# Performance work log

Measured on AMD Instinct MI355X. Metric: run time of the kernel, lower is better.

The kernel has to match this reference:

```python
import jax, jax.numpy as jnp
import numpy as np

B, S, HID = 2, 1024, 1024
H, P, D = 16, 2, 64
SCALE = 1.0 / np.sqrt(D)


def setup_inputs() -> dict:
    key = jax.random.key(0)
    ks = jax.random.split(key, 9)
    hidden_states = jax.random.normal(ks[0], (B, S, HID), dtype=jnp.float32)
    w_std = 0.02
    Wq = jax.random.normal(ks[1], (HID, HID), dtype=jnp.float32) * w_std
    Wk = jax.random.normal(ks[2], (HID, HID), dtype=jnp.float32) * w_std
    Wv = jax.random.normal(ks[3], (HID, HID), dtype=jnp.float32) * w_std
    Wo = jax.random.normal(ks[4], (HID, HID), dtype=jnp.float32) * w_std
    # alpha_* initialized as identity over heads, broadcast over pseudo dim, plus noise
    ident = jnp.broadcast_to(jnp.eye(H, dtype=jnp.float32)[:, :, None], (H, H, P))
    alpha_q = ident + 0.01 * jax.random.normal(ks[5], (H, H, P), dtype=jnp.float32)
    alpha_k = ident + 0.01 * jax.random.normal(ks[6], (H, H, P), dtype=jnp.float32)
    alpha_v = ident + 0.01 * jax.random.normal(ks[7], (H, H, P), dtype=jnp.float32)
    # collapse: (H, H*P), one-hot picking pseudo-head 0 of each head, plus noise
    collapse = jnp.zeros((H, H * P), dtype=jnp.float32)
    hi = jnp.arange(H)
    collapse = collapse.at[hi, hi * P].set(1.0)
    collapse = collapse + 0.01 * jax.random.normal(ks[8], (H, H * P), dtype=jnp.float32)
    return {"hidden_states": hidden_states, "Wq": Wq, "Wk": Wk, "Wv": Wv, "Wo": Wo,
            "alpha_q": alpha_q, "alpha_k": alpha_k, "alpha_v": alpha_v, "collapse": collapse}


def _iha_forward(x, Wq, Wk, Wv, Wo, alpha_q, alpha_k, alpha_v, collapse):
    b, s, _ = x.shape
    # projections (torch F.linear: x @ W^T), split into heads -> (b, H, s, D)
    def proj(W):
        return jnp.einsum('bse,fe->bsf', x, W).reshape(b, s, H, D).transpose(0, 2, 1, 3)
    q, k, v = proj(Wq), proj(Wk), proj(Wv)
    # head mixing: mhp,bmnd->bhpnd then merge pseudo into virtual seq (b,H,s*P,D)
    def mix_merge(alpha, t):
        t = jnp.einsum('mhp,bmnd->bhpnd', alpha, t)
        return t.transpose(0, 1, 3, 2, 4).reshape(b, H, s * P, D)
    q, k, v = mix_merge(alpha_q, q), mix_merge(alpha_k, k), mix_merge(alpha_v, v)
    # causal SDPA over virtual positions
    sv = s * P
    scores = jnp.einsum('bhqd,bhkd->bhqk', q, k) * jnp.asarray(SCALE, x.dtype)
    vpos = jnp.arange(sv)
    causal = vpos[:, None] >= vpos[None, :]
    scores = jnp.where(causal, scores, jnp.asarray(-jnp.inf, x.dtype))
    probs = jax.nn.softmax(scores, axis=-1)
    attn = jnp.einsum('bhqk,bhkd->bhqd', probs, v)  # (b, H, sv, D)
    # collapse pseudo heads: (b,H,s,P,D) -> (b,s,H*P,D) -> einsum with collapse
    attn = attn.reshape(b, H, s, P, D).transpose(0, 2, 1, 3, 4).reshape(b, s, H * P, D)
    attn = jnp.einsum('ho,bnod->bhnd', collapse, attn)  # (b, H, s, D)
    attn = attn.transpose(0, 2, 1, 3).reshape(b, s, HID)
    return jnp.einsum('bse,fe->bsf', attn, Wo)


def reference(hidden_states, Wq, Wk, Wv, Wo, alpha_q, alpha_k, alpha_v, collapse):
    return _iha_forward(hidden_states, Wq, Wk, Wv, Wo, alpha_q, alpha_k, alpha_v, collapse)
```

## Files before the change

### kernel.cpp

```cpp
#include <hip/hip_runtime.h>
#include <hip/hip_bf16.h>

#define B_    2
#define S_    1024
#define HID_  1024
#define H_    16
#define P_    2
#define D_    64
#define SV_   2048
#define NBH_  32
#define SCALE_LOG2E 0.18033688f

typedef __attribute__((ext_vector_type(8))) short short8;
typedef __attribute__((ext_vector_type(4))) short short4b;
typedef __attribute__((ext_vector_type(4))) float f32x4;

#if __has_builtin(__builtin_amdgcn_exp2f)
#define EXP2(x) __builtin_amdgcn_exp2f(x)
#else
#define EXP2(x) exp2f(x)
#endif

__device__ __forceinline__ unsigned short f2bf(float f) {
  union { float f; unsigned u; } v; v.f = f;
  unsigned r = v.u + 0x7fffu + ((v.u >> 16) & 1u);
  return (unsigned short)(r >> 16);
}
__device__ __forceinline__ unsigned pack_bf2(float a, float b) {
  __hip_bfloat162 h = __float22bfloat162_rn(make_float2(a, b));
  unsigned u; __builtin_memcpy(&u, &h, 4);
  return u;
}

__global__ __launch_bounds__(256) void prep_kernel(
    const float* __restrict__ x,
    const float* __restrict__ Wq, const float* __restrict__ Wk,
    const float* __restrict__ Wv, const float* __restrict__ Wo,
    const float* __restrict__ aq, const float* __restrict__ ak,
    const float* __restrict__ av, const float* __restrict__ coll,
    unsigned short* __restrict__ Xb, unsigned short* __restrict__ Weff,
    unsigned short* __restrict__ Woeff) {
  __shared__ float shbuf[1536];
  const int bid = blockIdx.x;
  const int tid = threadIdx.x;

  if (bid < 1024) {
    const int n4 = (B_ * S_ * HID_) / 4;
    int i = bid * 256 + tid;
    const int stride = 1024 * 256;
    for (; i < n4; i += stride) {
      float4 v = ((const float4*)x)[i];
      ushort4 o;
      o.x = f2bf(v.x); o.y = f2bf(v.y); o.z = f2bf(v.z); o.w = f2bf(v.w);
      ((ushort4*)Xb)[i] = o;
    }
  } else if (bid < 1216) {
    const int wb = bid - 1024;
    const int d = wb & 63;
    const int t = wb >> 6;
    const float* W = (t == 0) ? Wq : ((t == 1) ? Wk : Wv);
    const float* A = (t == 0) ? aq : ((t == 1) ? ak : av);
    float (*Al)[32] = (float (*)[32])shbuf;
    for (int idx = tid; idx < 512; idx += 256) Al[idx >> 5][idx & 31] = A[idx];
    __syncthreads();
    const int e = tid * 4;
    float wr[16][4];
#pragma unroll
    for (int m = 0; m < 16; ++m) {
      float4 v = *(const float4*)(W + (size_t)(m * 64 + d) * 1024 + e);
      wr[m][0] = v.x; wr[m][1] = v.y; wr[m][2] = v.z; wr[m][3] = v.w;
    }
    for (int hp = 0; hp < 32; ++hp) {
      float acc0 = 0.f, acc1 = 0.f, acc2 = 0.f, acc3 = 0.f;
#pragma unroll
      for (int m = 0; m < 16; ++m) {
        float al = Al[m][hp];
        acc0 += al * wr[m][0]; acc1 += al * wr[m][1];
        acc2 += al * wr[m][2]; acc3 += al * wr[m][3];
      }
      int r = (hp >> 1) * 128 + (hp & 1) * 64 + d;
      ushort4 ov;
      ov.x = f2bf(acc0); ov.y = f2bf(acc1); ov.z = f2bf(acc2); ov.w = f2bf(acc3);
      *(ushort4*)(Weff + ((size_t)t * 2048 + r) * 1024 + e) = ov;
    }
  } else {
    const int f = bid - 1216;
    float* wrow = shbuf;
    float* cl = shbuf + 1024;
    for (int idx = tid; idx < 512; idx += 256) cl[idx] = coll[idx];
    for (int idx = tid; idx < 1024; idx += 256) wrow[idx] = Wo[(size_t)f * 1024 + idx];
    __syncthreads();
    for (int idx = tid; idx < 2048; idx += 256) {
      int o = idx >> 6, d = idx & 63;
      float acc = 0.f;
#pragma unroll
      for (int h = 0; h < 16; ++h) acc += wrow[h * 64 + d] * cl[h * 32 + o];
      Woeff[(size_t)f * 2048 + idx] = f2bf(acc);
    }
  }
}

__global__ __launch_bounds__(256, 3) void qkv_gemm128(
    const unsigned short* __restrict__ Xb,
    const unsigned short* __restrict__ Weff,
    unsigned short* __restrict__ Qd, unsigned short* __restrict__ Kd,
    unsigned short* __restrict__ Vd) {
  __shared__ unsigned short As[3][128 * 32];
  __shared__ unsigned short Bs[3][128 * 32];
  constexpr int K = 1024, NT = 32;
  const int t = threadIdx.x;
  const int wave = t >> 6, lane = t & 63, lq = lane & 15, quad = lane >> 4;
  const int wm = wave >> 1, wn = wave & 1;
  const int z = blockIdx.z;
  const int row0 = blockIdx.x * 128, col0 = blockIdx.y * 128;
  const unsigned short* Ap = (z == 2) ? (Weff + (size_t)2 * 2048 * 1024) : Xb;
  const unsigned short* Bp = (z == 2) ? Xb : (Weff + (size_t)z * 2048 * 1024);

  const int srow = lane >> 2;
  const int sgr = (lane & 3) ^ ((lane >> 3) & 3);

  auto stage = [&](int kt, int buf) {
#pragma unroll
    for (int j = 0; j < 2; ++j) {
      const int rloc = wave * 32 + j * 16;
      const unsigned short* ga =
          Ap + (size_t)(row0 + rloc + srow) * K + kt * 32 + sgr * 8;
      __builtin_amdgcn_global_load_lds(
          (const __attribute__((address_space(1))) unsigned int*)ga,
          (__attribute__((address_space(3))) unsigned int*)(&As[buf][rloc * 32]),
          16, 0, 0);
      const unsigned short* gb =
          Bp + (size_t)(col0 + rloc + srow) * K + kt * 32 + sgr * 8;
      __builtin_amdgcn_global_load_lds(
          (const __attribute__((address_space(1))) unsigned int*)gb,
          (__attribute__((address_space(3))) unsigned int*)(&Bs[buf][rloc * 32]),
          16, 0, 0);
    }
  };

  f32x4 acc[4][4];
#pragma unroll
  for (int mi = 0; mi < 4; ++mi)
#pragma unroll
    for (int ni = 0; ni < 4; ++ni) acc[mi][ni] = (f32x4){0.f, 0.f, 0.f, 0.f};

  stage(0, 0);
  stage(1, 1);

  const int swz4 = (lq >> 1) & 3;

  for (int kt = 0; kt < NT; ++kt) {
    const int buf = kt % 3;
    if (kt + 1 < NT) {
      asm volatile("s_waitcnt vmcnt(4)" ::: "memory");
    } else {
      asm volatile("s_waitcnt vmcnt(0)" ::: "memory");
    }
    asm volatile("s_barrier" ::: "memory");
    if (kt + 2 < NT) stage(kt + 2, (kt + 2) % 3);

    const unsigned short* __restrict__ Ab = &As[buf][0];
    const unsigned short* __restrict__ Bb = &Bs[buf][0];
    short8 af[4], bf[4];
#pragma unroll
    for (int mi = 0; mi < 4; ++mi)
      af[mi] = *(const short8*)(
          Ab + (wm * 64 + mi * 16 + lq) * 32 + ((quad ^ swz4) * 8));
#pragma unroll
    for (int ni = 0; ni < 4; ++ni)
      bf[ni] = *(const short8*)(
          Bb + (wn * 64 + ni * 16 + lq) * 32 + ((quad ^ swz4) * 8));
    __builtin_amdgcn_s_setprio(1);
#pragma unroll
    for (int mi = 0; mi < 4; ++mi)
#pragma unroll
      for (int ni = 0; ni < 4; ++ni)
        acc[mi][ni] = __builtin_amdgcn_mfma_f32_16x16x32_bf16(
            af[mi], bf[ni], acc[mi][ni], 0, 0, 0);
    __builtin_amdgcn_s_setprio(0);
  }

#pragma unroll
  for (int mi = 0; mi < 4; ++mi) {
#pragma unroll
    for (int ni = 0; ni < 4; ++ni) {
#pragma unroll
      for (int i = 0; i < 4; ++i) {
        int grow = row0 + wm * 64 + mi * 16 + quad * 4 + i;
        int gcol = col0 + wn * 64 + ni * 16 + lq;
        float val = acc[mi][ni][i];
        if (z != 2) {
          if (z == 0) val *= SCALE_LOG2E;
          int b = grow >> 10, n = grow & 1023;
          int h = gcol >> 7, p = (gcol >> 6) & 1, d = gcol & 63;
          unsigned short* dst = (z == 0) ? Qd : Kd;
          dst[((size_t)((b * 16 + h) * 2048) + n * 2 + p) * 64 + d] = f2bf(val);
        } else {
          int h = grow >> 7, p = (grow >> 6) & 1, d = grow & 63;
          int b = gcol >> 10, n = gcol & 1023;
          Vd[((size_t)((b * 16 + h) * 64 + d)) * 2048 + n * 2 + p] = f2bf(val);
        }
      }
    }
  }
}

__global__ __launch_bounds__(256) void gemm64p(
    const unsigned short* __restrict__ A,
    const unsigned short* __restrict__ Bbase,
    float* __restrict__ Cf) {
  __shared__ unsigned short As[3][64 * 64];
  __shared__ unsigned short Bs[3][64 * 64];
  constexpr int K = 2048, N = 1024, NT = 32;
  const int t = threadIdx.x;
  const int wave = t >> 6, lane = t & 63, lrow = lane & 15, quad = lane >> 4;
  const int wm = wave >> 1, wn = wave & 1;
  const int row0 = blockIdx.x * 64, col0 = blockIdx.y * 64;
  const int srow8 = lane >> 3;
  const int sslot = (lane & 7) ^ srow8;
  const int swz = lrow & 7;

  auto stage = [&](int kt, int buf) {
#pragma unroll
    for (int j = 0; j < 2; ++j) {
      const int rloc = wave * 16 + j * 8;
      const unsigned short* ga =
          A + (size_t)(row0 + rloc + srow8) * K + kt * 64 + sslot * 8;
      __builtin_amdgcn_global_load_lds(
          (const __attribute__((address_space(1))) unsigned int*)ga,
          (__attribute__((address_space(3))) unsigned int*)(&As[buf][rloc * 64]),
          16, 0, 0);
      const unsigned short* gb =
          Bbase + (size_t)(col0 + rloc + srow8) * K + kt * 64 + sslot * 8;
      __builtin_amdgcn_global_load_lds(
          (const __attribute__((address_space(1))) unsigned int*)gb,
          (__attribute__((address_space(3))) unsigned int*)(&Bs[buf][rloc * 64]),
          16, 0, 0);
    }
  };

  f32x4 acc[2][2];
#pragma unroll
  for (int mi = 0; mi < 2; ++mi)
#pragma unroll
    for (int ni = 0; ni < 2; ++ni) acc[mi][ni] = (f32x4){0.f, 0.f, 0.f, 0.f};

  stage(0, 0);
  stage(1, 1);

  for (int kt = 0; kt < NT; ++kt) {
    const int buf = kt % 3;
    if (kt < NT - 1) {
      asm volatile("s_waitcnt vmcnt(4)" ::: "memory");
    } else {
      asm volatile("s_waitcnt vmcnt(0)" ::: "memory");
    }
    asm volatile("s_barrier" ::: "memory");
    if (kt + 2 < NT) stage(kt + 2, (kt + 2) % 3);

    const unsigned short* __restrict__ Ab = &As[buf][0];
    const unsigned short* __restrict__ Bb = &Bs[buf][0];
    short8 af[2][2], bf[2][2];
#pragma unroll
    for (int mi = 0; mi < 2; ++mi)
#pragma unroll
      for (int ks = 0; ks < 2; ++ks)
        af[mi][ks] = *(const short8*)(
            Ab + (wm * 32 + mi * 16 + lrow) * 64 + (((ks * 4 + quad) ^ swz) * 8));
#pragma unroll
    for (int ni = 0; ni < 2; ++ni)
#pragma unroll
      for (int ks = 0; ks < 2; ++ks)
        bf[ni][ks] = *(const short8*)(
            Bb + (wn * 32 + ni * 16 + lrow) * 64 + (((ks * 4 + quad) ^ swz) * 8));
    __builtin_amdgcn_s_setprio(1);
#pragma unroll
    for (int mi = 0; mi < 2; ++mi)
#pragma unroll
      for (int ni = 0; ni < 2; ++ni) {
        acc[mi][ni] = __builtin_amdgcn_mfma_f32_16x16x32_bf16(
            af[mi][0], bf[ni][0], acc[mi][ni], 0, 0, 0);
        acc[mi][ni] = __builtin_amdgcn_mfma_f32_16x16x32_bf16(
            af[mi][1], bf[ni][1], acc[mi][ni], 0, 0, 0);
      }
    __builtin_amdgcn_s_setprio(0);
  }

#pragma unroll
  for (int mi = 0; mi < 2; ++mi)
#pragma unroll
    for (int ni = 0; ni < 2; ++ni)
#pragma unroll
      for (int i = 0; i < 4; ++i) {
        int grow = row0 + wm * 32 + mi * 16 + quad * 4 + i;
        int gcol = col0 + wn * 32 + ni * 16 + lrow;
        Cf[(size_t)grow * N + gcol] = acc[mi][ni][i];
      }
}

__global__ __launch_bounds__(256, 3) void attn_kernel(
    const unsigned short* __restrict__ Qv, const unsigned short* __restrict__ Kv,
    const unsigned short* __restrict__ Vt, unsigned short* __restrict__ Aov) {
  __shared__ unsigned short Ks[3][4096];
  __shared__ unsigned short Vs[3][4096];
  const int bh = blockIdx.x;
  const int yy = blockIdx.y;
  const int qt = (yy < 16) ? yy : (47 - yy);
  const int t = threadIdx.x;
  const int w = t >> 6, lane = t & 63, lq = lane & 15, quad = lane >> 4;
  const int l3 = lq & 7;

  const unsigned short* Qh = Qv + (size_t)bh * SV_ * D_;
  const unsigned short* Kh = Kv + (size_t)bh * SV_ * D_;
  const unsigned short* Vh = Vt + (size_t)bh * D_ * SV_;

  const int qrow = qt * 64 + w * 16 + lq;
  short8 bq0 = *(const short8*)(Qh + (size_t)qrow * 64 + quad * 8);
  short8 bq1 = *(const short8*)(Qh + (size_t)qrow * 64 + 32 + quad * 8);

  const int sg = (lane & 7) ^ ((lane >> 3) & 7);
  const int r0 = w * 16 + (lane >> 3);
  const unsigned short* Kg0 = Kh + r0 * 64 + sg * 8;
  const unsigned short* Vg0 = Vh + (size_t)r0 * SV_ + sg * 8;
  const int lds0 = w * 1024;
  const int lds1 = lds0 + 512;

  auto stage = [&](int kt) {
    const int buf = kt % 3;
    const unsigned short* kg = Kg0 + kt * 4096;
    const unsigned short* vg = Vg0 + kt * 64;
    __builtin_amdgcn_global_load_lds(
        (const __attribute__((address_space(1))) unsigned int*)kg,
        (__attribute__((address_space(3))) unsigned int*)(&Ks[buf][lds0]), 16, 0, 0);
    __builtin_amdgcn_global_load_lds(
        (const __attribute__((address_space(1))) unsigned int*)(kg + 8 * 64),
        (__attribute__((address_space(3))) unsigned int*)(&Ks[buf][lds1]), 16, 0, 0);
    __builtin_amdgcn_global_load_lds(
        (const __attribute__((address_space(1))) unsigned int*)vg,
        (__attribute__((address_space(3))) unsigned int*)(&Vs[buf][lds0]), 16, 0, 0);
    __builtin_amdgcn_global_load_lds(
        (const __attribute__((address_space(1))) unsigned int*)(vg + (size_t)8 * SV_),
        (__attribute__((address_space(3))) unsigned int*)(&Vs[buf][lds1]), 16, 0, 0);
  };

  float l_sum = 0.f;
  f32x4 o_acc[4];
#pragma unroll
  for (int nd = 0; nd < 4; ++nd) o_acc[nd] = (f32x4){0.f, 0.f, 0.f, 0.f};

  const int nt = qt + 1;
  stage(0);
  if (nt > 1) stage(1);

  for (int kt = 0; kt < nt; ++kt) {
    const int buf = kt % 3;
    if (kt + 1 < nt) {
      asm volatile("s_waitcnt vmcnt(4)" ::: "memory");
    } else {
      asm volatile("s_waitcnt vmcnt(0)" ::: "memory");
    }
    asm volatile("s_barrier" ::: "memory");
    if (kt + 2 < nt) stage(kt + 2);

    const unsigned short* Kb = Ks[buf];
    short8 ka[4][2];
#pragma unroll
    for (int t4 = 0; t4 < 4; ++t4)
#pragma unroll
      for (int c = 0; c < 2; ++c)
        ka[t4][c] = *(const short8*)(Kb + (t4 * 16 + lq) * 64 + (((c * 4 + quad) ^ l3) * 8));

    f32x4 s[4];
#pragma unroll
    for (int t4 = 0; t4 < 4; ++t4) {
      f32x4 z = (f32x4){0.f, 0.f, 0.f, 0.f};
      z = __builtin_amdgcn_mfma_f32_16x16x32_bf16(ka[t4][0], bq0, z, 0, 0, 0);
      s[t4] = __builtin_amdgcn_mfma_f32_16x16x32_bf16(ka[t4][1], bq1, z, 0, 0, 0);
    }

    const bool diag = (kt == qt);
    const int kc0 = kt * 64 + quad * 4;
    const unsigned short* Vb = Vs[buf];
    float rs = 0.f;
    __builtin_amdgcn_s_setprio(1);
#pragma unroll
    for (int t4 = 0; t4 < 4; ++t4) {
      float p0 = EXP2(s[t4][0]), p1 = EXP2(s[t4][1]);
      float p2 = EXP2(s[t4][2]), p3 = EXP2(s[t4][3]);
      if (diag) {
        const int kc = kc0 + t4 * 16;
        if (kc + 0 > qrow) p0 = 0.f;
        if (kc + 1 > qrow) p1 = 0.f;
        if (kc + 2 > qrow) p2 = 0.f;
        if (kc + 3 > qrow) p3 = 0.f;
      }
      rs += (p0 + p1) + (p2 + p3);
      unsigned ww[2];
      ww[0] = pack_bf2(p0, p1);
      ww[1] = pack_bf2(p2, p3);
      short4b pb;
      __builtin_memcpy(&pb, ww, 8);
      const int cg = t4 * 2 + (quad >> 1);
      const int vcol = ((cg ^ l3) * 8) + (quad & 1) * 4;
#pragma unroll
      for (int nd = 0; nd < 4; ++nd) {
        short4b va4;
        __builtin_memcpy(&va4, Vb + (nd * 16 + lq) * 64 + vcol, 8);
        o_acc[nd] = __builtin_amdgcn_mfma_f32_16x16x16bf16_1k(va4, pb,
                                                              o_acc[nd], 0, 0, 0);
      }
    }
    __builtin_amdgcn_s_setprio(0);
    l_sum += rs;
  }

  l_sum += __shfl_xor(l_sum, 16);
  l_sum += __shfl_xor(l_sum, 32);

  const int b = bh >> 4, h = bh & 15;
  const float inv = 1.0f / l_sum;
  const int n = qrow >> 1, p = qrow & 1;
  unsigned short* dst = Aov + ((size_t)(b * 1024 + n)) * 2048 + (h * 2 + p) * 64;
#pragma unroll
  for (int nd = 0; nd < 4; ++nd) {
    uint2 dw;
    dw.x = pack_bf2(o_acc[nd][0] * inv, o_acc[nd][1] * inv);
    dw.y = pack_bf2(o_acc[nd][2] * inv, o_acc[nd][3] * inv);
    *(uint2*)(dst + nd * 16 + quad * 4) = dw;
  }
}

extern "C" void kernel_launch(void* const* d_in, const int* in_sizes, int n_in,
                              void* d_out, int out_size, void* d_ws, size_t ws_size,
                              hipStream_t stream) {
  (void)in_sizes; (void)n_in; (void)out_size; (void)ws_size;
  const float* x    = (const float*)d_in[0];
  const float* Wq   = (const float*)d_in[1];
  const float* Wk   = (const float*)d_in[2];
  const float* Wv   = (const float*)d_in[3];
  const float* Wo   = (const float*)d_in[4];
  const float* aq   = (const float*)d_in[5];
  const float* ak   = (const float*)d_in[6];
  const float* av   = (const float*)d_in[7];
  const float* coll = (const float*)d_in[8];
  float* out = (float*)d_out;

  char* ws = (char*)d_ws;
  const size_t MB = 1024 * 1024;
  unsigned short* Xb    = (unsigned short*)(ws);
  unsigned short* Woeff = (unsigned short*)(ws + 4 * MB);
  unsigned short* Weff  = (unsigned short*)(ws + 8 * MB);
  unsigned short* Qv    = (unsigned short*)(ws + 20 * MB);
  unsigned short* Kv    = (unsigned short*)(ws + 28 * MB);
  unsigned short* Vt    = (unsigned short*)(ws + 36 * MB);
  unsigned short* Aov   = (unsigned short*)(ws + 8 * MB);

  prep_kernel<<<dim3(2240), dim3(256), 0, stream>>>(
      x, Wq, Wk, Wv, Wo, aq, ak, av, coll, Xb, Weff, Woeff);
  qkv_gemm128<<<dim3(16, 16, 3), dim3(256), 0, stream>>>(Xb, Weff, Qv, Kv, Vt);
  attn_kernel<<<dim3(32, 32), dim3(256), 0, stream>>>(Qv, Kv, Vt, Aov);
  gemm64p<<<dim3(32, 16), dim3(256), 0, stream>>>(Aov, Woeff, out);
}
```

Baseline: 189.1 us.

## Process two query tiles per attention block to reuse staged K/V

Each attention workgroup now handles 128 query rows (two 64-row tiles) instead of 64, so every K/V tile staged into LDS feeds two sets of score and PV MFMAs. The grid is halved and the causal tile mapping is adjusted to match. The aim is to cut global-to-LDS traffic and barrier overhead per unit of work. In exchange, register pressure roughly doubles for the accumulators (launch bounds lowered to 2 waves per SIMD), there are half as many blocks to balance across CUs, and the first tile does a skipped extra iteration.

```diff
diff --git a/kernel.cpp b/kernel.cpp
--- a/kernel.cpp
+++ b/kernel.cpp
@@ -298,14 +298,14 @@
       }
 }
 
-__global__ __launch_bounds__(256, 3) void attn_kernel(
+__global__ __launch_bounds__(256, 2) void attn_kernel(
     const unsigned short* __restrict__ Qv, const unsigned short* __restrict__ Kv,
     const unsigned short* __restrict__ Vt, unsigned short* __restrict__ Aov) {
   __shared__ unsigned short Ks[3][4096];
   __shared__ unsigned short Vs[3][4096];
   const int bh = blockIdx.x;
   const int yy = blockIdx.y;
-  const int qt = (yy < 16) ? yy : (47 - yy);
+  const int qt = (yy < 8) ? yy : (23 - yy);
   const int t = threadIdx.x;
   const int w = t >> 6, lane = t & 63, lq = lane & 15, quad = lane >> 4;
   const int l3 = lq & 7;
@@ -314,9 +314,12 @@
   const unsigned short* Kh = Kv + (size_t)bh * SV_ * D_;
   const unsigned short* Vh = Vt + (size_t)bh * D_ * SV_;
 
-  const int qrow = qt * 64 + w * 16 + lq;
-  short8 bq0 = *(const short8*)(Qh + (size_t)qrow * 64 + quad * 8);
-  short8 bq1 = *(const short8*)(Qh + (size_t)qrow * 64 + 32 + quad * 8);
+  const int qrow0 = qt * 128 + w * 16 + lq;
+  const int qrow1 = qrow0 + 64;
+  short8 bq0_0 = *(const short8*)(Qh + (size_t)qrow0 * 64 + quad * 8);
+  short8 bq1_0 = *(const short8*)(Qh + (size_t)qrow0 * 64 + 32 + quad * 8);
+  short8 bq0_1 = *(const short8*)(Qh + (size_t)qrow1 * 64 + quad * 8);
+  short8 bq1_1 = *(const short8*)(Qh + (size_t)qrow1 * 64 + 32 + quad * 8);
 
   const int sg = (lane & 7) ^ ((lane >> 3) & 7);
   const int r0 = w * 16 + (lane >> 3);
@@ -343,14 +346,17 @@
         (__attribute__((address_space(3))) unsigned int*)(&Vs[buf][lds1]), 16, 0, 0);
   };
 
-  float l_sum = 0.f;
-  f32x4 o_acc[4];
-#pragma unroll
-  for (int nd = 0; nd < 4; ++nd) o_acc[nd] = (f32x4){0.f, 0.f, 0.f, 0.f};
-
-  const int nt = qt + 1;
+  float l_sum0 = 0.f, l_sum1 = 0.f;
+  f32x4 o_acc0[4], o_acc1[4];
+#pragma unroll
+  for (int nd = 0; nd < 4; ++nd) {
+    o_acc0[nd] = (f32x4){0.f, 0.f, 0.f, 0.f};
+    o_acc1[nd] = (f32x4){0.f, 0.f, 0.f, 0.f};
+  }
+
+  const int nt = 2 * qt + 2;
   stage(0);
-  if (nt > 1) stage(1);
+  stage(1);
 
   for (int kt = 0; kt < nt; ++kt) {
     const int buf = kt % 3;
@@ -370,63 +376,122 @@
       for (int c = 0; c < 2; ++c)
         ka[t4][c] = *(const short8*)(Kb + (t4 * 16 + lq) * 64 + (((c * 4 + quad) ^ l3) * 8));
 
-    f32x4 s[4];
-#pragma unroll
-    for (int t4 = 0; t4 < 4; ++t4) {
-      f32x4 z = (f32x4){0.f, 0.f, 0.f, 0.f};
-      z = __builtin_amdgcn_mfma_f32_16x16x32_bf16(ka[t4][0], bq0, z, 0, 0, 0);
-      s[t4] = __builtin_amdgcn_mfma_f32_16x16x32_bf16(ka[t4][1], bq1, z, 0, 0, 0);
-    }
-
-    const bool diag = (kt == qt);
+    const unsigned short* Vb = Vs[buf];
     const int kc0 = kt * 64 + quad * 4;
-    const unsigned short* Vb = Vs[buf];
-    float rs = 0.f;
     __builtin_amdgcn_s_setprio(1);
-#pragma unroll
-    for (int t4 = 0; t4 < 4; ++t4) {
-      float p0 = EXP2(s[t4][0]), p1 = EXP2(s[t4][1]);
-      float p2 = EXP2(s[t4][2]), p3 = EXP2(s[t4][3]);
-      if (diag) {
-        const int kc = kc0 + t4 * 16;
-        if (kc + 0 > qrow) p0 = 0.f;
-        if (kc + 1 > qrow) p1 = 0.f;
-        if (kc + 2 > qrow) p2 = 0.f;
-        if (kc + 3 > qrow) p3 = 0.f;
-      }
-      rs += (p0 + p1) + (p2 + p3);
-      unsigned ww[2];
-      ww[0] = pack_bf2(p0, p1);
-      ww[1] = pack_bf2(p2, p3);
-      short4b pb;
-      __builtin_memcpy(&pb, ww, 8);
-      const int cg = t4 * 2 + (quad >> 1);
-      const int vcol = ((cg ^ l3) * 8) + (quad & 1) * 4;
-#pragma unroll
-      for (int nd = 0; nd < 4; ++nd) {
-        short4b va4;
-        __builtin_memcpy(&va4, Vb + (nd * 16 + lq) * 64 + vcol, 8);
-        o_acc[nd] = __builtin_amdgcn_mfma_f32_16x16x16bf16_1k(va4, pb,
-                                                              o_acc[nd], 0, 0, 0);
-      }
-    }
+
+    if (kt <= 2 * qt) {
+      f32x4 s[4];
+#pragma unroll
+      for (int t4 = 0; t4 < 4; ++t4) {
+        f32x4 zz = (f32x4){0.f, 0.f, 0.f, 0.f};
+        zz = __builtin_amdgcn_mfma_f32_16x16x32_bf16(ka[t4][0], bq0_0, zz, 0, 0, 0);
+        s[t4] = __builtin_amdgcn_mfma_f32_16x16x32_bf16(ka[t4][1], bq1_0, zz, 0, 0, 0);
+      }
+      const bool diag = (kt == 2 * qt);
+      float rs = 0.f;
+#pragma unroll
+      for (int t4 = 0; t4 < 4; ++t4) {
+        float p0 = EXP2(s[t4][0]), p1 = EXP2(s[t4][1]);
+        float p2 = EXP2(s[t4][2]), p3 = EXP2(s[t4][3]);
+        if (diag) {
+          const int kc = kc0 + t4 * 16;
+          if (kc + 0 > qrow0) p0 = 0.f;
+          if (kc + 1 > qrow0) p1 = 0.f;
+          if (kc + 2 > qrow0) p2 = 0.f;
+          if (kc + 3 > qrow0) p3 = 0.f;
+        }
+        rs += (p0 + p1) + (p2 + p3);
+        unsigned ww[2];
+        ww[0] = pack_bf2(p0, p1);
+        ww[1] = pack_bf2(p2, p3);
+        short4b pb;
+        __builtin_memcpy(&pb, ww, 8);
+        const int cg = t4 * 2 + (quad >> 1);
+        const int vcol = ((cg ^ l3) * 8) + (quad & 1) * 4;
+#pragma unroll
+        for (int nd = 0; nd < 4; ++nd) {
+          short4b va4;
+          __builtin_memcpy(&va4, Vb + (nd * 16 + lq) * 64 + vcol, 8);
+          o_acc0[nd] = __builtin_amdgcn_mfma_f32_16x16x16bf16_1k(va4, pb,
+                                                                 o_acc0[nd], 0, 0, 0);
+        }
+      }
+      l_sum0 += rs;
+    }
+
+    {
+      f32x4 s[4];
+#pragma unroll
+      for (int t4 = 0; t4 < 4; ++t4) {
+        f32x4 zz = (f32x4){0.f, 0.f, 0.f, 0.f};
+        zz = __builtin_amdgcn_mfma_f32_16x16x32_bf16(ka[t4][0], bq0_1, zz, 0, 0, 0);
+        s[t4] = __builtin_amdgcn_mfma_f32_16x16x32_bf16(ka[t4][1], bq1_1, zz, 0, 0, 0);
+      }
+      const bool diag = (kt == 2 * qt + 1);
+      float rs = 0.f;
+#pragma unroll
+      for (int t4 = 0; t4 < 4; ++t4) {
+        float p0 = EXP2(s[t4][0]), p1 = EXP2(s[t4][1]);
+        float p2 = EXP2(s[t4][2]), p3 = EXP2(s[t4][3]);
+        if (diag) {
+          const int kc = kc0 + t4 * 16;
+          if (kc + 0 > qrow1) p0 = 0.f;
+          if (kc + 1 > qrow1) p1 = 0.f;
+          if (kc + 2 > qrow1) p2 = 0.f;
+          if (kc + 3 > qrow1) p3 = 0.f;
+        }
+        rs += (p0 + p1) + (p2 + p3);
+        unsigned ww[2];
+        ww[0] = pack_bf2(p0, p1);
+        ww[1] = pack_bf2(p2, p3);
+        short4b pb;
+        __builtin_memcpy(&pb, ww, 8);
+        const int cg = t4 * 2 + (quad >> 1);
+        const int vcol = ((cg ^ l3) * 8) + (quad & 1) * 4;
+#pragma unroll
+        for (int nd = 0; nd < 4; ++nd) {
+          short4b va4;
+          __builtin_memcpy(&va4, Vb + (nd * 16 + lq) * 64 + vcol, 8);
+          o_acc1[nd] = __builtin_amdgcn_mfma_f32_16x16x16bf16_1k(va4, pb,
+                                                                 o_acc1[nd], 0, 0, 0);
+        }
+      }
+      l_sum1 += rs;
+    }
+
     __builtin_amdgcn_s_setprio(0);
-    l_sum += rs;
-  }
-
-  l_sum += __shfl_xor(l_sum, 16);
-  l_sum += __shfl_xor(l_sum, 32);
+  }
+
+  l_sum0 += __shfl_xor(l_sum0, 16);
+  l_sum0 += __shfl_xor(l_sum0, 32);
+  l_sum1 += __shfl_xor(l_sum1, 16);
+  l_sum1 += __shfl_xor(l_sum1, 32);
 
   const int b = bh >> 4, h = bh & 15;
-  const float inv = 1.0f / l_sum;
-  const int n = qrow >> 1, p = qrow & 1;
-  unsigned short* dst = Aov + ((size_t)(b * 1024 + n)) * 2048 + (h * 2 + p) * 64;
-#pragma unroll
-  for (int nd = 0; nd < 4; ++nd) {
-    uint2 dw;
-    dw.x = pack_bf2(o_acc[nd][0] * inv, o_acc[nd][1] * inv);
-    dw.y = pack_bf2(o_acc[nd][2] * inv, o_acc[nd][3] * inv);
-    *(uint2*)(dst + nd * 16 + quad * 4) = dw;
+  {
+    const float inv = 1.0f / l_sum0;
+    const int n = qrow0 >> 1, p = qrow0 & 1;
+    unsigned short* dst = Aov + ((size_t)(b * 1024 + n)) * 2048 + (h * 2 + p) * 64;
+#pragma unroll
+    for (int nd = 0; nd < 4; ++nd) {
+      uint2 dw;
+      dw.x = pack_bf2(o_acc0[nd][0] * inv, o_acc0[nd][1] * inv);
+      dw.y = pack_bf2(o_acc0[nd][2] * inv, o_acc0[nd][3] * inv);
+      *(uint2*)(dst + nd * 16 + quad * 4) = dw;
+    }
+  }
+  {
+    const float inv = 1.0f / l_sum1;
+    const int n = qrow1 >> 1, p = qrow1 & 1;
+    unsigned short* dst = Aov + ((size_t)(b * 1024 + n)) * 2048 + (h * 2 + p) * 64;
+#pragma unroll
+    for (int nd = 0; nd < 4; ++nd) {
+      uint2 dw;
+      dw.x = pack_bf2(o_acc1[nd][0] * inv, o_acc1[nd][1] * inv);
+      dw.y = pack_bf2(o_acc1[nd][2] * inv, o_acc1[nd][3] * inv);
+      *(uint2*)(dst + nd * 16 + quad * 4) = dw;
+    }
   }
 }
 
@@ -458,6 +523,6 @@
   prep_kernel<<<dim3(2240), dim3(256), 0, stream>>>(
       x, Wq, Wk, Wv, Wo, aq, ak, av, coll, Xb, Weff, Woeff);
   qkv_gemm128<<<dim3(16, 16, 3), dim3(256), 0, stream>>>(Xb, Weff, Qv, Kv, Vt);
-  attn_kernel<<<dim3(32, 32), dim3(256), 0, stream>>>(Qv, Kv, Vt, Aov);
+  attn_kernel<<<dim3(32, 16), dim3(256), 0, stream>>>(Qv, Kv, Vt, Aov);
   gemm64p<<<dim3(32, 16), dim3(256), 0, stream>>>(Aov, Woeff, out);
 }
```

New measurement: 198.8 us. 1.05x slower.
